# Optimization experiments

Measured on AMD Instinct MI355X. Metric: run time of the kernel, lower is better.

## Reference

```python
import jax, jax.numpy as jnp
import numpy as np

B, N, F_, CI, C, CO = 2, 1024, 2048, 3, 80, 128
NB = 15          # DirResNet blocks
Q = C // 4


def _graph_bn(x, g, b, eps=1e-5):
    # BatchNorm over channels with stats over (batch, nodes) -- training-mode batch stats
    mu = jnp.mean(x, axis=(0, 1), keepdims=True)
    var = jnp.var(x, axis=(0, 1), keepdims=True)
    return (x - mu) * jax.lax.rsqrt(var + eps) * g + b


def _graph_conv(L, x, W0, W1, bias):
    # GraphConv with k=1: linear on [x, L @ x]
    return x @ W0 + jnp.einsum('bnm,bmc->bnc', L, x) @ W1 + bias


def _forward(inputs, L, Di, DiA, mask,
             conv1_W0, conv1_W1, conv1_b,
             rn_bn0_g, rn_bn0_b, rn_fc0_W, rn_fc0_b,
             rn_bn1_g, rn_bn1_b, rn_fc1_W, rn_fc1_b,
             bn1_g, bn1_b, bn2_g, bn2_b, bn3_g, bn3_b,
             conv2_W0, conv2_W1, conv2_b):
    v = _graph_conv(L, inputs, conv1_W0, conv1_W1, conv1_b)      # [B,N,C]
    f = jnp.zeros((B, F_, C), v.dtype)
    z = jnp.zeros_like(v)
    carry = (f, f, v, z, z)  # [f, tmp_f, v, tmp_v, tmp_v]

    def block(carry, p):
        f, tmp_f, v, tv0, tv1 = carry
        g0, b0, W0, c0, g1, b1, W1, c1 = p
        # Dirac: vertices -> faces (quaternion reshape: [B,N,C] -> [B,4N,C/4])
        Dv = jnp.matmul(Di, v.reshape(B, 4 * N, Q)).reshape(B, F_, C)
        x = jnp.concatenate([f, Dv], axis=-1)                    # [B,F,2C]
        f_new = jax.nn.elu(_graph_bn(x, g0, b0) @ W0 + c0) + tmp_f
        # Adjoint Dirac: faces -> vertices
        Df = jnp.matmul(DiA, f_new.reshape(B, 4 * F_, Q)).reshape(B, N, C)
        y = jnp.concatenate([v, Df], axis=-1)                    # [B,N,2C]
        v_new = jax.nn.elu(_graph_bn(y, g1, b1) @ W1 + c1) + tv0
        return (f_new, f, v_new, v, tv0), None

    carry, _ = jax.lax.scan(
        block, carry,
        (rn_bn0_g, rn_bn0_b, rn_fc0_W, rn_fc0_b,
         rn_bn1_g, rn_bn1_b, rn_fc1_W, rn_fc1_b))
    _, _, v2, v1, v0 = carry
    v = jax.nn.elu(_graph_bn(v2, bn1_g, bn1_b)
                   + _graph_bn(v1, bn2_g, bn2_b)
                   + _graph_bn(v0, bn3_g, bn3_b))
    # Dropout2d: identity (eval mode / deterministic reference)
    v = _graph_conv(L, v, conv2_W0, conv2_W1, conv2_b)           # [B,N,CO]
    out = (v * mask).sum(axis=1) / mask.sum(axis=1)              # masked mean pool -> [B,CO]
    return out


def setup_inputs() -> dict:
    key = jax.random.key(0)
    ks = jax.random.split(key, 32)
    s = 0.05
    d = {
        'inputs': jax.random.normal(ks[0], (B, N, CI), jnp.float32),
        'L': jax.random.normal(ks[1], (B, N, N), jnp.float32) / np.float32(np.sqrt(N)),
        'Di': jax.random.normal(ks[2], (B, 4 * F_, 4 * N), jnp.float32) / np.float32(np.sqrt(4 * N)),
        'DiA': jax.random.normal(ks[3], (B, 4 * N, 4 * F_), jnp.float32) / np.float32(np.sqrt(4 * F_)),
        'mask': (jax.random.uniform(ks[4], (B, N, 1)) > 0.2).astype(jnp.float32),
        'conv1_W0': jax.random.normal(ks[5], (CI, C), jnp.float32) * s,
        'conv1_W1': jax.random.normal(ks[6], (CI, C), jnp.float32) * s,
        'conv1_b': jax.random.normal(ks[7], (C,), jnp.float32) * s,
        'rn_bn0_g': 1.0 + 0.1 * jax.random.normal(ks[8], (NB, 2 * C), jnp.float32),
        'rn_bn0_b': s * jax.random.normal(ks[9], (NB, 2 * C), jnp.float32),
        'rn_fc0_W': jax.random.normal(ks[10], (NB, 2 * C, C), jnp.float32) * s,
        'rn_fc0_b': jax.random.normal(ks[11], (NB, C), jnp.float32) * s,
        'rn_bn1_g': 1.0 + 0.1 * jax.random.normal(ks[12], (NB, 2 * C), jnp.float32),
        'rn_bn1_b': s * jax.random.normal(ks[13], (NB, 2 * C), jnp.float32),
        'rn_fc1_W': jax.random.normal(ks[14], (NB, 2 * C, C), jnp.float32) * s,
        'rn_fc1_b': jax.random.normal(ks[15], (NB, C), jnp.float32) * s,
        'bn1_g': 1.0 + 0.1 * jax.random.normal(ks[16], (C,), jnp.float32),
        'bn1_b': s * jax.random.normal(ks[17], (C,), jnp.float32),
        'bn2_g': 1.0 + 0.1 * jax.random.normal(ks[18], (C,), jnp.float32),
        'bn2_b': s * jax.random.normal(ks[19], (C,), jnp.float32),
        'bn3_g': 1.0 + 0.1 * jax.random.normal(ks[20], (C,), jnp.float32),
        'bn3_b': s * jax.random.normal(ks[21], (C,), jnp.float32),
        'conv2_W0': jax.random.normal(ks[22], (C, CO), jnp.float32) * s,
        'conv2_W1': jax.random.normal(ks[23], (C, CO), jnp.float32) * s,
        'conv2_b': jax.random.normal(ks[24], (CO,), jnp.float32) * s,
    }
    return d


def reference(inputs, L, Di, DiA, mask,
              conv1_W0, conv1_W1, conv1_b,
              rn_bn0_g, rn_bn0_b, rn_fc0_W, rn_fc0_b,
              rn_bn1_g, rn_bn1_b, rn_fc1_W, rn_fc1_b,
              bn1_g, bn1_b, bn2_g, bn2_b, bn3_g, bn3_b,
              conv2_W0, conv2_W1, conv2_b):
    return _forward(inputs, L, Di, DiA, mask,
                    conv1_W0, conv1_W1, conv1_b,
                    rn_bn0_g, rn_bn0_b, rn_fc0_W, rn_fc0_b,
                    rn_bn1_g, rn_bn1_b, rn_fc1_W, rn_fc1_b,
                    bn1_g, bn1_b, bn2_g, bn2_b, bn3_g, bn3_b,
                    conv2_W0, conv2_W1, conv2_b)
```

## Files before the change

kernel.cpp:

```cpp
#include <hip/hip_runtime.h>
#include <cstdint>

#define BB 2
#define NN 1024
#define FF 2048
#define CC 80
#define C2 160
#define NB_ 15
#define ROWS_X (BB*FF)
#define ROWS_Y (BB*NN)
#define WTP 168

typedef __attribute__((ext_vector_type(8))) _Float16 half8;
typedef __attribute__((ext_vector_type(4))) _Float16 half4;
typedef __attribute__((ext_vector_type(4))) float f32x4;

__device__ __forceinline__ void softbar() {
  __builtin_amdgcn_sched_barrier(0);
  asm volatile("s_waitcnt lgkmcnt(0)" ::: "memory");
  __builtin_amdgcn_s_barrier();
  __builtin_amdgcn_sched_barrier(0);
}

__global__ __launch_bounds__(256) void k_conv1(
    const float* __restrict__ inp, const float* __restrict__ L,
    const float* __restrict__ W0, const float* __restrict__ W1,
    const float* __restrict__ bias, float* __restrict__ v,
    float4* __restrict__ vstat)
{
  int bx = blockIdx.x;
  int b = bx >> 6, rb = bx & 63;
  int row0 = rb * 16;
  __shared__ float red[256][3];
  __shared__ float lx[16][3];
  __shared__ float st[16][2][CC];
  int t = threadIdx.x;
  int rloc = t >> 4, sl = t & 15;
  const float* Lrow = L + ((size_t)b*NN + row0 + rloc) * NN;
  const float* ipb  = inp + (size_t)b*NN*3;
  float a0=0.f,a1=0.f,a2=0.f;
  for (int m = sl; m < NN; m += 16) {
    float lv = Lrow[m];
    a0 = fmaf(lv, ipb[m*3+0], a0);
    a1 = fmaf(lv, ipb[m*3+1], a1);
    a2 = fmaf(lv, ipb[m*3+2], a2);
  }
  red[t][0]=a0; red[t][1]=a1; red[t][2]=a2;
  __syncthreads();
  if (t < 48) {
    int row = t/3, ci = t%3;
    float s=0.f;
    for (int s2=0; s2<16; ++s2) s += red[row*16+s2][ci];
    lx[row][ci]=s;
  }
  __syncthreads();
  for (int o = t; o < 16*CC; o += 256) {
    int row = o/CC, c = o%CC;
    const float* ir = inp + ((size_t)b*NN + row0 + row)*3;
    float val = bias[c];
    #pragma unroll
    for (int ci=0; ci<3; ++ci)
      val += ir[ci]*W0[ci*CC+c] + lx[row][ci]*W1[ci*CC+c];
    v[((size_t)b*NN + row0 + row)*CC + c] = val;
    st[row][0][c] = val;
    st[row][1][c] = val*val;
  }
  __syncthreads();
  if (t < 40) {
    float s0=0.f,q0=0.f,s1=0.f,q1=0.f;
    for (int row=0; row<16; ++row){
      s0+=st[row][0][2*t];   q0+=st[row][1][2*t];
      s1+=st[row][0][2*t+1]; q1+=st[row][1][2*t+1];
    }
    vstat[(size_t)bx*40 + t] = make_float4(s0,q0,s1,q1);
  }
}

__device__ __forceinline__ unsigned pkh(float a, float b){
  _Float16 ha = (_Float16)a, hb = (_Float16)b;
  unsigned short ua = __builtin_bit_cast(unsigned short, ha);
  unsigned short ub = __builtin_bit_cast(unsigned short, hb);
  return (unsigned)ua | ((unsigned)ub << 16);
}
__global__ __launch_bounds__(256) void k_cvt(
    const float* __restrict__ src, uint4* __restrict__ dst, size_t n8)
{
  size_t i = (size_t)blockIdx.x*256 + threadIdx.x;
  size_t stride = (size_t)gridDim.x*256;
  for (; i < n8; i += stride) {
    const float4* s = (const float4*)src + i*2;
    float4 f0 = s[0], f1 = s[1];
    uint4 o;
    o.x = pkh(f0.x,f0.y); o.y = pkh(f0.z,f0.w);
    o.z = pkh(f1.x,f1.y); o.w = pkh(f1.z,f1.w);
    dst[i] = o;
  }
}

__global__ __launch_bounds__(256) __attribute__((amdgpu_waves_per_eu(2,2)))
void k_dirac_mfma(
    const _Float16* __restrict__ A, const float* __restrict__ x,
    float* __restrict__ y, float4* __restrict__ stat, int M, int K)
{
  int b = blockIdx.y;
  A += (size_t)b*M*K; x += (size_t)b*(size_t)K*20; y += (size_t)b*(size_t)M*20;
  __shared__ _Float16 xT[2][2][32][264];
  __shared__ float cb_[2][8][64];
  __shared__ float stS[2][CC], stQ[2][CC];
  int t = threadIdx.x, lane = t & 63, w = t >> 6;
  int rw = w & 1, kh = w >> 1;
  int row0 = blockIdx.x*32 + rw*16;
  int cl = lane & 15, cg = lane >> 4;
  int KH = K >> 1;
  f32x4 acc0 = {0.f,0.f,0.f,0.f}, acc1 = {0.f,0.f,0.f,0.f};
  const float4* xv = (const float4*)x;
  int nchunk = KH >> 8;
  const _Float16* Abase = A + (size_t)(row0 + cl)*K + (size_t)kh*KH + cg*8;

  for (int i = t; i < 2*2*12*264; i += 256) {
    int bb = i / (2*12*264);
    int rem = i - bb*(2*12*264);
    int hh = rem / (12*264);
    int r2 = rem - hh*(12*264);
    xT[bb][hh][20 + r2/264][r2 % 264] = (_Float16)0.f;
  }
  {
    float4 s0[5], s1[5];
    #pragma unroll
    for (int i=0;i<5;++i){ s0[i]=xv[(size_t)t*5+i]; s1[i]=xv[((size_t)KH+t)*5+i]; }
    #pragma unroll
    for (int i=0;i<5;++i){
      xT[0][0][4*i+0][t]=(_Float16)s0[i].x; xT[0][0][4*i+1][t]=(_Float16)s0[i].y;
      xT[0][0][4*i+2][t]=(_Float16)s0[i].z; xT[0][0][4*i+3][t]=(_Float16)s0[i].w;
      xT[0][1][4*i+0][t]=(_Float16)s1[i].x; xT[0][1][4*i+1][t]=(_Float16)s1[i].y;
      xT[0][1][4*i+2][t]=(_Float16)s1[i].z; xT[0][1][4*i+3][t]=(_Float16)s1[i].w;
    }
  }
  half8 a_cur[8];
  #pragma unroll
  for (int ks=0;ks<8;++ks) a_cur[ks] = *(const half8*)(Abase + ks*32);
  __syncthreads();

  for (int c=0; c<nchunk; ++c) {
    int cur = c & 1;
    bool more = (c+1 < nchunk);
    float4 s0[5], s1[5];
    half8 a_nxt[8];
    if (more) {
      size_t k0 = (size_t)(c+1)*256 + t;
      #pragma unroll
      for (int i=0;i<5;++i){ s0[i]=xv[k0*5+i]; s1[i]=xv[(k0+KH)*5+i]; }
      const _Float16* An = Abase + (size_t)(c+1)*256;
      #pragma unroll
      for (int ks=0;ks<8;++ks) a_nxt[ks] = *(const half8*)(An + ks*32);
    }
    #pragma unroll
    for (int ks=0;ks<8;++ks) {
      half8 b0 = *(const half8*)(&xT[cur][kh][cl     ][ks*32 + cg*8]);
      half8 b1 = *(const half8*)(&xT[cur][kh][16 + cl][ks*32 + cg*8]);
      acc0 = __builtin_amdgcn_mfma_f32_16x16x32_f16(a_cur[ks], b0, acc0, 0,0,0);
      acc1 = __builtin_amdgcn_mfma_f32_16x16x32_f16(a_cur[ks], b1, acc1, 0,0,0);
    }
    if (more) {
      #pragma unroll
      for (int i=0;i<5;++i){
        xT[cur^1][0][4*i+0][t]=(_Float16)s0[i].x; xT[cur^1][0][4*i+1][t]=(_Float16)s0[i].y;
        xT[cur^1][0][4*i+2][t]=(_Float16)s0[i].z; xT[cur^1][0][4*i+3][t]=(_Float16)s0[i].w;
        xT[cur^1][1][4*i+0][t]=(_Float16)s1[i].x; xT[cur^1][1][4*i+1][t]=(_Float16)s1[i].y;
        xT[cur^1][1][4*i+2][t]=(_Float16)s1[i].z; xT[cur^1][1][4*i+3][t]=(_Float16)s1[i].w;
      }
      #pragma unroll
      for (int ks=0;ks<8;++ks) a_cur[ks] = a_nxt[ks];
    }
    softbar();
  }

  if (kh == 1) {
    #pragma unroll
    for (int j=0;j<4;++j){ cb_[rw][j][lane]=acc0[j]; cb_[rw][4+j][lane]=acc1[j]; }
  }
  __syncthreads();
  if (kh == 0) {
    #pragma unroll
    for (int j=0;j<4;++j){ acc0[j]+=cb_[rw][j][lane]; acc1[j]+=cb_[rw][4+j][lane]; }
    #pragma unroll
    for (int j=0;j<4;++j) {
      float v = acc0[j];
      y[(size_t)(row0 + 4*cg + j)*20 + cl] = v;
      float s = v, sq = v*v;
      s  += __shfl_xor(s,16);  s  += __shfl_xor(s,32);
      sq += __shfl_xor(sq,16); sq += __shfl_xor(sq,32);
      if (cg==0) { stS[rw][j*20+cl]=s; stQ[rw][j*20+cl]=sq; }
    }
    #pragma unroll
    for (int j=0;j<4;++j) {
      float v = acc1[j];
      if (cl < 4) y[(size_t)(row0 + 4*cg + j)*20 + 16 + cl] = v;
      float s = v, sq = v*v;
      s  += __shfl_xor(s,16);  s  += __shfl_xor(s,32);
      sq += __shfl_xor(sq,16); sq += __shfl_xor(sq,32);
      if (cg==0 && cl<4) { stS[rw][j*20+16+cl]=s; stQ[rw][j*20+16+cl]=sq; }
    }
  }
  __syncthreads();
  int slot = blockIdx.y*gridDim.x + blockIdx.x;
  if (t < 40) {
    float4 o;
    o.x = stS[0][2*t]  +stS[1][2*t];
    o.y = stQ[0][2*t]  +stQ[1][2*t];
    o.z = stS[0][2*t+1]+stS[1][2*t+1];
    o.w = stQ[0][2*t+1]+stQ[1][2*t+1];
    stat[(size_t)slot*40 + t] = o;
  }
}

__global__ __launch_bounds__(256) __attribute__((amdgpu_waves_per_eu(2,2)))
void k_dirac_f32(
    const float* __restrict__ A, const float* __restrict__ x,
    float* __restrict__ y, float4* __restrict__ stat, int M, int K)
{
  const int DR = 4;
  int b = blockIdx.y;
  A += (size_t)b*M*K; x += (size_t)b*(size_t)K*20; y += (size_t)b*(size_t)M*20;
  __shared__ float xs[2][20][256];
  __shared__ float stS[4][CC], stQ[4][CC];
  int t = threadIdx.x, lane = t & 63, w = t >> 6;
  int row0 = blockIdx.x*(4*DR) + w*DR;
  float acc[DR][20];
  #pragma unroll
  for (int r=0;r<DR;++r)
    #pragma unroll
    for (int q=0;q<20;++q) acc[r][q]=0.f;
  const float4* xv = (const float4*)x;
  int nchunk = K >> 8;
  const float* Abase = A + (size_t)row0*K + (lane<<2);
  {
    float4 s0[5];
    #pragma unroll
    for (int i=0;i<5;++i) s0[i] = xv[(size_t)t*5 + i];
    #pragma unroll
    for (int i=0;i<5;++i) {
      xs[0][4*i+0][t]=s0[i].x; xs[0][4*i+1][t]=s0[i].y;
      xs[0][4*i+2][t]=s0[i].z; xs[0][4*i+3][t]=s0[i].w;
    }
  }
  float4 a[DR];
  #pragma unroll
  for (int r=0;r<DR;++r) a[r] = *(const float4*)(Abase + (size_t)r*K);
  __syncthreads();
  for (int c=0; c<nchunk; ++c) {
    int cur = c & 1;
    bool more = (c+1 < nchunk);
    float4 st[5];
    if (more) {
      size_t kb = (size_t)(c+1)*256 + t;
      #pragma unroll
      for (int i=0;i<5;++i) st[i] = xv[kb*5 + i];
    }
    float4 af[DR];
    #pragma unroll
    for (int r=0;r<DR;++r) af[r] = a[r];
    if (more) {
      const float* An = Abase + (size_t)(c+1)*256;
      #pragma unroll
      for (int r=0;r<DR;++r) a[r] = *(const float4*)(An + (size_t)r*K);
    }
    #pragma unroll
    for (int q=0;q<20;++q) {
      float4 xq = *(const float4*)(&xs[cur][q][lane<<2]);
      #pragma unroll
      for (int r=0;r<DR;++r) {
        acc[r][q] = fmaf(af[r].x, xq.x, acc[r][q]);
        acc[r][q] = fmaf(af[r].y, xq.y, acc[r][q]);
        acc[r][q] = fmaf(af[r].z, xq.z, acc[r][q]);
        acc[r][q] = fmaf(af[r].w, xq.w, acc[r][q]);
      }
    }
    if (more) {
      #pragma unroll
      for (int i=0;i<5;++i) {
        xs[cur^1][4*i+0][t]=st[i].x; xs[cur^1][4*i+1][t]=st[i].y;
        xs[cur^1][4*i+2][t]=st[i].z; xs[cur^1][4*i+3][t]=st[i].w;
      }
    }
    __syncthreads();
  }
  #pragma unroll
  for (int r=0;r<DR;++r) {
    #pragma unroll
    for (int q=0;q<20;++q) {
      float s = acc[r][q];
      s += __shfl_xor(s, 1);  s += __shfl_xor(s, 2);
      s += __shfl_xor(s, 4);  s += __shfl_xor(s, 8);
      s += __shfl_xor(s, 16); s += __shfl_xor(s, 32);
      acc[r][q]=s;
    }
    if (lane==0) {
      float4* yp = (float4*)(y + (size_t)(row0+r)*20);
      yp[0] = make_float4(acc[r][0],acc[r][1],acc[r][2],acc[r][3]);
      yp[1] = make_float4(acc[r][4],acc[r][5],acc[r][6],acc[r][7]);
      yp[2] = make_float4(acc[r][8],acc[r][9],acc[r][10],acc[r][11]);
      yp[3] = make_float4(acc[r][12],acc[r][13],acc[r][14],acc[r][15]);
      yp[4] = make_float4(acc[r][16],acc[r][17],acc[r][18],acc[r][19]);
    }
  }
  if (lane == 0) {
    #pragma unroll
    for (int r=0;r<DR;++r)
      #pragma unroll
      for (int q=0;q<20;++q) {
        float v0 = acc[r][q];
        stS[w][r*20+q] = v0;
        stQ[w][r*20+q] = v0*v0;
      }
  }
  __syncthreads();
  int slot = blockIdx.y*gridDim.x + blockIdx.x;
  if (t < 40) {
    float4 o;
    o.x = stS[0][2*t]+stS[1][2*t]+stS[2][2*t]+stS[3][2*t];
    o.y = stQ[0][2*t]+stQ[1][2*t]+stQ[2][2*t]+stQ[3][2*t];
    o.z = stS[0][2*t+1]+stS[1][2*t+1]+stS[2][2*t+1]+stS[3][2*t+1];
    o.w = stQ[0][2*t+1]+stQ[1][2*t+1]+stQ[2][2*t+1]+stQ[3][2*t+1];
    stat[(size_t)slot*40 + t] = o;
  }
}

__global__ __launch_bounds__(320) void k_fc(
    const float* __restrict__ p1, const float* __restrict__ p2,
    const float4* __restrict__ sp1, int ns1,
    const float4* __restrict__ sp2, int ns2,
    const float* __restrict__ g, const float* __restrict__ bb,
    const float* __restrict__ W, const float* __restrict__ cb,
    const float* add, float* out,
    float4* __restrict__ statout, int rows, float invrows)
{
  __shared__ _Float16 Wt[80*WTP];
  __shared__ _Float16 xh[16*WTP];
  __shared__ float ad[2][C2];
  __shared__ float bpl[CC];
  __shared__ float4 pst[2][2][40];
  __shared__ float stS[CC], stQ[CC];
  int t = threadIdx.x;
  int lane = t & 63, wv = t >> 6;
  int cl = lane & 15, cg = lane >> 4;
  int r0 = blockIdx.x * 16;

  if (t < 160) {
    int p = t % 40, s = (t/40) & 1, h = t/80;
    const float4* sp = s ? sp2 : sp1;
    int ns = s ? ns2 : ns1;
    int half = ns >> 1;
    const float4* base = sp + (size_t)(h*half)*40 + p;
    float4 acc = {0.f,0.f,0.f,0.f};
    int i=0;
    for (; i+8<=half; i+=8) {
      float4 v[8];
      #pragma unroll
      for (int j=0;j<8;++j) v[j] = base[(size_t)(i+j)*40];
      #pragma unroll
      for (int j=0;j<8;++j){ acc.x+=v[j].x; acc.y+=v[j].y; acc.z+=v[j].z; acc.w+=v[j].w; }
    }
    for (; i<half; ++i){
      float4 v = base[(size_t)i*40];
      acc.x+=v.x; acc.y+=v.y; acc.z+=v.z; acc.w+=v.w;
    }
    pst[h][s][p] = acc;
  } else {
    int t2 = t - 160;
    #pragma unroll
    for (int i=0;i<20;++i) {
      int f4 = t2 + i*160;
      float4 w4 = ((const float4*)W)[f4];
      int c2 = f4/20, c = (f4%20)*4;
      Wt[(c+0)*WTP + c2] = (_Float16)w4.x;
      Wt[(c+1)*WTP + c2] = (_Float16)w4.y;
      Wt[(c+2)*WTP + c2] = (_Float16)w4.z;
      Wt[(c+3)*WTP + c2] = (_Float16)w4.w;
    }
  }
  __syncthreads();

  half8 bfr[5];
  #pragma unroll
  for (int ks=0;ks<5;++ks)
    bfr[ks] = *(const half8*)(&Wt[(wv*16+cl)*WTP + ks*32 + cg*8]);
  if (t < C2) {
    int s = (t < CC) ? 0 : 1;
    int chl = (t < CC) ? t : t - CC;
    int p = chl >> 1, e = chl & 1;
    float4 a0 = pst[0][s][p], a1 = pst[1][s][p];
    float S = e ? (a0.z + a1.z) : (a0.x + a1.x);
    float Q = e ? (a0.w + a1.w) : (a0.y + a1.y);
    float mean = S*invrows;
    float var  = fmaf(-mean, mean, Q*invrows);
    float aa   = g[t]*rsqrtf(var + 1e-5f);
    ad[0][t]=aa; ad[1][t]= bb[t] - mean*aa;
  }
  __syncthreads();

  #pragma unroll
  for (int i=0;i<2;++i) {
    int f4 = t + i*320;
    if (f4 < 640) {
      int row = f4/40, cq = (f4%40)*4;
      const float* src = (cq < 80) ? (p1 + (size_t)(r0+row)*CC + cq)
                                   : (p2 + (size_t)(r0+row)*CC + cq - 80);
      float4 x4 = *(const float4*)src;
      half4 h4;
      h4[0]=(_Float16)(x4.x*ad[0][cq+0]); h4[1]=(_Float16)(x4.y*ad[0][cq+1]);
      h4[2]=(_Float16)(x4.z*ad[0][cq+2]); h4[3]=(_Float16)(x4.w*ad[0][cq+3]);
      *(half4*)(&xh[row*WTP + cq]) = h4;
    }
  }
  if (t < CC) {
    float s = cb[t];
    #pragma unroll
    for (int ks=0;ks<20;++ks) {
      half8 w8 = *(const half8*)(&Wt[t*WTP + ks*8]);
      #pragma unroll
      for (int j=0;j<8;++j) s = fmaf(ad[1][ks*8+j], (float)w8[j], s);
    }
    bpl[t]=s;
  }
  __syncthreads();

  half8 afr[5];
  #pragma unroll
  for (int ks=0;ks<5;++ks)
    afr[ks] = *(const half8*)(&xh[cl*WTP + ks*32 + cg*8]);
  f32x4 acc = {0.f,0.f,0.f,0.f};
  #pragma unroll
  for (int ks=0;ks<5;++ks)
    acc = __builtin_amdgcn_mfma_f32_16x16x32_f16(afr[ks], bfr[ks], acc, 0,0,0);
  float ss=0.f, sq=0.f;
  int col = wv*16 + cl;
  #pragma unroll
  for (int j=0;j<4;++j) {
    int row = r0 + 4*cg + j;
    float val = acc[j] + bpl[col];
    val = val>0.f ? val : expm1f(val);
    val += add[(size_t)row*CC + col];
    out[(size_t)row*CC + col] = val;
    ss += val; sq = fmaf(val,val,sq);
  }
  ss += __shfl_xor(ss,16); ss += __shfl_xor(ss,32);
  sq += __shfl_xor(sq,16); sq += __shfl_xor(sq,32);
  if (cg==0) { stS[col]=ss; stQ[col]=sq; }
  __syncthreads();
  if (t < 40)
    statout[(size_t)blockIdx.x*40 + t] = make_float4(stS[2*t], stQ[2*t], stS[2*t+1], stQ[2*t+1]);
}

__global__ __launch_bounds__(256) void k_final(
    const float* __restrict__ v2, const float* __restrict__ v1, const float* __restrict__ v0,
    const float4* __restrict__ s2, const float4* __restrict__ s1, const float4* __restrict__ s0,
    const float* __restrict__ g1, const float* __restrict__ b1,
    const float* __restrict__ g2, const float* __restrict__ b2,
    const float* __restrict__ g3, const float* __restrict__ b3,
    float* __restrict__ vf, int ns)
{
  __shared__ float A[3][CC], D[3][CC];
  __shared__ float4 pf[2][3][40];
  int t = threadIdx.x;
  if (t < 240) {
    int p = t % 40, s = (t/40) % 3, h = t/120;
    const float4* sp = s==0 ? s2 : (s==1 ? s1 : s0);
    int half = ns >> 1;
    const float4* base = sp + (size_t)(h*half)*40 + p;
    float4 acc = {0.f,0.f,0.f,0.f};
    int i=0;
    for (; i+8<=half; i+=8) {
      float4 v[8];
      #pragma unroll
      for (int j=0;j<8;++j) v[j] = base[(size_t)(i+j)*40];
      #pragma unroll
      for (int j=0;j<8;++j){ acc.x+=v[j].x; acc.y+=v[j].y; acc.z+=v[j].z; acc.w+=v[j].w; }
    }
    for (; i<half; ++i){
      float4 v = base[(size_t)i*40];
      acc.x+=v.x; acc.y+=v.y; acc.z+=v.z; acc.w+=v.w;
    }
    pf[h][s][p] = acc;
  }
  __syncthreads();
  if (t < 240) {
    int set = t/80, chl = t%80, p = chl>>1, e = chl&1;
    const float* gg  = set==0? g1 : (set==1? g2 : g3);
    const float* bbp = set==0? b1 : (set==1? b2 : b3);
    float4 a0 = pf[0][set][p], a1 = pf[1][set][p];
    float S = e ? (a0.z + a1.z) : (a0.x + a1.x);
    float Q = e ? (a0.w + a1.w) : (a0.y + a1.y);
    float mean = S*(1.f/ROWS_Y);
    float var  = fmaf(-mean,mean,Q*(1.f/ROWS_Y));
    float aa   = gg[chl]*rsqrtf(var+1e-5f);
    A[set][chl]=aa; D[set][chl]=bbp[chl]-mean*aa;
  }
  __syncthreads();
  for (size_t idx = (size_t)blockIdx.x*256 + t; idx < (size_t)ROWS_Y*CC; idx += (size_t)gridDim.x*256) {
    int c = (int)(idx % CC);
    float val = fmaf(v2[idx],A[0][c],D[0][c]) + fmaf(v1[idx],A[1][c],D[1][c]) + fmaf(v0[idx],A[2][c],D[2][c]);
    vf[idx] = val>0.f? val : expm1f(val);
  }
}

__global__ __launch_bounds__(256) void k_w(
    const float* __restrict__ mask, const float* __restrict__ L, float* __restrict__ w)
{
  int bx = blockIdx.x;
  int b = bx >> 4, n0 = (bx & 15) * 64;
  int t = threadIdx.x;
  int ks = t >> 6;
  __shared__ float red[4][64];
  float acc=0.f;
  const float* Lb = L + (size_t)b*NN*NN;
  const float* mb = mask + b*NN;
  int n = n0 + (t & 63);
  for (int k = ks*256; k < ks*256+256; k+=8) {
    float mv[8], lv[8];
    #pragma unroll
    for (int j=0;j<8;++j){ mv[j]=mb[k+j]; lv[j]=Lb[(size_t)(k+j)*NN + n]; }
    #pragma unroll
    for (int j=0;j<8;++j) acc = fmaf(mv[j], lv[j], acc);
  }
  red[ks][t&63]=acc;
  __syncthreads();
  if (t < 64) w[b*NN + n0 + t] = red[0][t]+red[1][t]+red[2][t]+red[3][t];
}

__global__ __launch_bounds__(256) void k_pool(
    const float* __restrict__ vf, const float* __restrict__ mask,
    const float* __restrict__ w, float* __restrict__ part)
{
  int bx = blockIdx.x;
  int b = bx >> 3, slab = bx & 7;
  int t = threadIdx.x, c = t%CC, rs = t/CC;
  __shared__ float st[3][2][CC];
  if (t<240) {
    float a1=0.f,a2=0.f;
    for (int r = rs; r < 128; r += 3) {
      int row = slab*128 + r;
      float val = vf[((size_t)b*NN + row)*CC + c];
      a1 = fmaf(mask[b*NN+row], val, a1);
      a2 = fmaf(w[b*NN+row],    val, a2);
    }
    st[rs][0][c]=a1; st[rs][1][c]=a2;
  }
  __syncthreads();
  if (t<CC) {
    part[((b*8+slab)*2+0)*CC+t] = st[0][0][t]+st[1][0][t]+st[2][0][t];
    part[((b*8+slab)*2+1)*CC+t] = st[0][1][t]+st[1][1][t]+st[2][1][t];
  }
}

__global__ __launch_bounds__(256) void k_out(
    const float* __restrict__ part, const float* __restrict__ mask,
    const float* __restrict__ W0, const float* __restrict__ W1,
    const float* __restrict__ b2, float* __restrict__ outp)
{
  __shared__ float pl[2][2][CC];
  __shared__ float msred[2][128];
  __shared__ float ms[2];
  int t = threadIdx.x;
  {
    int b = t >> 7, k0 = t & 127;
    float m[8];
    #pragma unroll
    for (int j=0;j<8;++j) m[j] = mask[b*NN + k0 + j*128];
    msred[b][k0] = ((m[0]+m[1])+(m[2]+m[3]))+((m[4]+m[5])+(m[6]+m[7]));
  }
  if (t < 160) {
    int b = t/CC, c = t%CC;
    float v1[8], v2[8];
    #pragma unroll
    for (int slab=0; slab<8; ++slab){
      v1[slab] = part[((b*8+slab)*2+0)*CC+c];
      v2[slab] = part[((b*8+slab)*2+1)*CC+c];
    }
    float s1=0.f,s2=0.f;
    #pragma unroll
    for (int slab=0;slab<8;++slab){ s1+=v1[slab]; s2+=v2[slab]; }
    pl[b][0][c]=s1; pl[b][1][c]=s2;
  }
  __syncthreads();
  if (t < 2) {
    float s=0.f;
    for (int k=0;k<128;++k) s += msred[t][k];
    ms[t]=s;
  }
  __syncthreads();
  int b = t >> 7, co = t & 127;
  float acc = 0.f;
  for (int c=0;c<CC;c+=8) {
    float w0[8], w1[8];
    #pragma unroll
    for (int j=0;j<8;++j){ w0[j]=W0[(c+j)*128+co]; w1[j]=W1[(c+j)*128+co]; }
    #pragma unroll
    for (int j=0;j<8;++j) acc += pl[b][0][c+j]*w0[j] + pl[b][1][c+j]*w1[j];
  }
  outp[t] = acc/ms[b] + b2[co];
}

extern "C" void kernel_launch(void* const* d_in, const int* in_sizes, int n_in,
                              void* d_out, int out_size, void* d_ws, size_t ws_size,
                              hipStream_t stream)
{
  const float* inp  = (const float*)d_in[0];
  const float* L    = (const float*)d_in[1];
  const float* Di   = (const float*)d_in[2];
  const float* DiA  = (const float*)d_in[3];
  const float* mask = (const float*)d_in[4];
  const float* c1W0 = (const float*)d_in[5];
  const float* c1W1 = (const float*)d_in[6];
  const float* c1b  = (const float*)d_in[7];
  const float* bn0g = (const float*)d_in[8];
  const float* bn0b = (const float*)d_in[9];
  const float* fc0W = (const float*)d_in[10];
  const float* fc0b = (const float*)d_in[11];
  const float* bn1g = (const float*)d_in[12];
  const float* bn1b = (const float*)d_in[13];
  const float* fc1W = (const float*)d_in[14];
  const float* fc1b = (const float*)d_in[15];
  const float* fbn1g= (const float*)d_in[16];
  const float* fbn1b= (const float*)d_in[17];
  const float* fbn2g= (const float*)d_in[18];
  const float* fbn2b= (const float*)d_in[19];
  const float* fbn3g= (const float*)d_in[20];
  const float* fbn3b= (const float*)d_in[21];
  const float* c2W0 = (const float*)d_in[22];
  const float* c2W1 = (const float*)d_in[23];
  const float* c2b  = (const float*)d_in[24];

  float* ws = (float*)d_ws;
  size_t off = 0;
  auto alloc = [&](size_t n)->float* { float* p = ws + off; off += (n + 63) & ~(size_t)63; return p; };
  const size_t STFL = (size_t)1024*40*4;
  float* vb[3];   for (int i=0;i<3;++i) vb[i]   = alloc((size_t)BB*NN*CC);
  float* fb[2];   for (int i=0;i<2;++i) fb[i]   = alloc((size_t)BB*FF*CC);
  float* Dv       = alloc((size_t)BB*FF*CC);
  float* Df       = alloc((size_t)BB*NN*CC);
  float4* vstat[3];for (int i=0;i<3;++i) vstat[i]= (float4*)alloc(STFL);
  float4* fstat[2];for (int i=0;i<2;++i) fstat[i]= (float4*)alloc(STFL);
  float4* dvstat  = (float4*)alloc(STFL);
  float4* dfstat  = (float4*)alloc(STFL);
  float* vf       = alloc((size_t)BB*NN*CC);
  float* wv       = alloc((size_t)BB*NN);
  float* part     = alloc((size_t)16*2*CC);
  const size_t nDi = (size_t)BB*(4*FF)*(4*NN);
  _Float16* Dih  = (_Float16*)alloc(nDi/2);
  _Float16* DiAh = (_Float16*)alloc(nDi/2);
  bool usebf = (off*sizeof(float) <= ws_size);

  hipMemsetAsync(fb[0],    0, (size_t)BB*FF*CC*4, stream);
  hipMemsetAsync(fb[1],    0, (size_t)BB*FF*CC*4, stream);
  hipMemsetAsync(vb[1],    0, (size_t)BB*NN*CC*4, stream);
  hipMemsetAsync(fstat[0], 0, (size_t)256*40*16, stream);

  if (usebf) {
    k_cvt<<<4096,256,0,stream>>>(Di,  (uint4*)Dih,  nDi/8);
    k_cvt<<<4096,256,0,stream>>>(DiA, (uint4*)DiAh, nDi/8);
  }

  k_conv1<<<128,256,0,stream>>>(inp, L, c1W0, c1W1, c1b, vb[0], vstat[0]);

  int nsDv = usebf ? 512 : 1024;
  int nsDf = usebf ? 256 : 512;
  int cur=0, p1=1, p2=2, fcur=0, fs=0;
  for (int it=0; it<NB_; ++it) {
    if (usebf) k_dirac_mfma<<<dim3(256,2),256,0,stream>>>(Dih, vb[cur], Dv, dvstat, 4*FF, 4*NN);
    else       k_dirac_f32 <<<dim3(512,2),256,0,stream>>>(Di,  vb[cur], Dv, dvstat, 4*FF, 4*NN);
    k_fc<<<ROWS_X/16,320,0,stream>>>(fb[fcur], Dv, fstat[fs],256, dvstat,nsDv,
        bn0g+(size_t)it*C2, bn0b+(size_t)it*C2, fc0W+(size_t)it*C2*CC, fc0b+(size_t)it*CC,
        fb[1-fcur], fb[1-fcur], fstat[1-fs], ROWS_X, 1.f/ROWS_X);
    fcur = 1-fcur; fs = 1-fs;
    if (usebf) k_dirac_mfma<<<dim3(128,2),256,0,stream>>>(DiAh, fb[fcur], Df, dfstat, 4*NN, 4*FF);
    else       k_dirac_f32 <<<dim3(256,2),256,0,stream>>>(DiA,  fb[fcur], Df, dfstat, 4*NN, 4*FF);
    k_fc<<<ROWS_Y/16,320,0,stream>>>(vb[cur], Df, vstat[cur],128, dfstat,nsDf,
        bn1g+(size_t)it*C2, bn1b+(size_t)it*C2, fc1W+(size_t)it*C2*CC, fc1b+(size_t)it*CC,
        vb[p1], vb[p2], vstat[p2], ROWS_Y, 1.f/ROWS_Y);
    int tmp=p2; p2=p1; p1=cur; cur=tmp;
  }

  k_final<<<128,256,0,stream>>>(vb[cur],vb[p1],vb[p2], vstat[cur],vstat[p1],vstat[p2],
      fbn1g,fbn1b,fbn2g,fbn2b,fbn3g,fbn3b, vf, 128);
  k_w<<<32,256,0,stream>>>(mask, L, wv);
  k_pool<<<16,256,0,stream>>>(vf, mask, wv, part);
  k_out<<<1,256,0,stream>>>(part, mask, c2W0, c2W1, c2b, (float*)d_out);
}
```

Before: 1.966 ms.

## Fuse fp32-to-fp16 Dirac conversion into first MFMA pass and widen adjoint grid

Drops the two standalone conversion kernels. On the first block iteration the Dirac MFMA kernel reads the fp32 operator directly, converts it to fp16 in registers, uses it, and writes the fp16 copy back for later iterations. The adjoint Dirac kernel is templated to use 128-thread blocks holding a single 16-row tile, which doubles its grid so more CUs are busy, and the stats slot count is updated to match. In exchange the first iteration loses the register prefetch of A (loads are synchronous) and has to read fp32 and write fp16 in-line.

```diff
diff --git a/kernel.cpp b/kernel.cpp
--- a/kernel.cpp
+++ b/kernel.cpp
@@ -76,48 +76,35 @@
   }
 }
 
-__device__ __forceinline__ unsigned pkh(float a, float b){
-  _Float16 ha = (_Float16)a, hb = (_Float16)b;
-  unsigned short ua = __builtin_bit_cast(unsigned short, ha);
-  unsigned short ub = __builtin_bit_cast(unsigned short, hb);
-  return (unsigned)ua | ((unsigned)ub << 16);
-}
-__global__ __launch_bounds__(256) void k_cvt(
-    const float* __restrict__ src, uint4* __restrict__ dst, size_t n8)
-{
-  size_t i = (size_t)blockIdx.x*256 + threadIdx.x;
-  size_t stride = (size_t)gridDim.x*256;
-  for (; i < n8; i += stride) {
-    const float4* s = (const float4*)src + i*2;
-    float4 f0 = s[0], f1 = s[1];
-    uint4 o;
-    o.x = pkh(f0.x,f0.y); o.y = pkh(f0.z,f0.w);
-    o.z = pkh(f1.x,f1.y); o.w = pkh(f1.z,f1.w);
-    dst[i] = o;
-  }
-}
-
-__global__ __launch_bounds__(256) __attribute__((amdgpu_waves_per_eu(2,2)))
+template<int WR, bool CVT>
+__global__ __launch_bounds__(WR*128) __attribute__((amdgpu_waves_per_eu(2,2)))
 void k_dirac_mfma(
-    const _Float16* __restrict__ A, const float* __restrict__ x,
+    const void* __restrict__ Ain, _Float16* __restrict__ Aout,
+    const float* __restrict__ x,
     float* __restrict__ y, float4* __restrict__ stat, int M, int K)
 {
+  constexpr int NT  = WR*128;
+  constexpr int RPT = 256/NT;
   int b = blockIdx.y;
-  A += (size_t)b*M*K; x += (size_t)b*(size_t)K*20; y += (size_t)b*(size_t)M*20;
+  x += (size_t)b*(size_t)K*20; y += (size_t)b*(size_t)M*20;
+  const _Float16* Ah = (const _Float16*)Ain + (size_t)b*M*K;
+  const float*    Af = (const float*)Ain    + (size_t)b*M*K;
+  _Float16* Ao = CVT ? (Aout + (size_t)b*M*K) : nullptr;
   __shared__ _Float16 xT[2][2][32][264];
-  __shared__ float cb_[2][8][64];
-  __shared__ float stS[2][CC], stQ[2][CC];
+  __shared__ float cb_[WR][8][64];
+  __shared__ float stS[WR][CC], stQ[WR][CC];
   int t = threadIdx.x, lane = t & 63, w = t >> 6;
-  int rw = w & 1, kh = w >> 1;
-  int row0 = blockIdx.x*32 + rw*16;
+  int rw = (WR==2) ? (w & 1) : 0;
+  int kh = (WR==2) ? (w >> 1) : w;
+  int row0 = blockIdx.x*(16*WR) + rw*16;
   int cl = lane & 15, cg = lane >> 4;
   int KH = K >> 1;
   f32x4 acc0 = {0.f,0.f,0.f,0.f}, acc1 = {0.f,0.f,0.f,0.f};
   const float4* xv = (const float4*)x;
   int nchunk = KH >> 8;
-  const _Float16* Abase = A + (size_t)(row0 + cl)*K + (size_t)kh*KH + cg*8;
-
-  for (int i = t; i < 2*2*12*264; i += 256) {
+  size_t aoff = (size_t)(row0 + cl)*K + (size_t)kh*KH + cg*8;
+
+  for (int i = t; i < 2*2*12*264; i += NT) {
     int bb = i / (2*12*264);
     int rem = i - bb*(2*12*264);
     int hh = rem / (12*264);
@@ -125,34 +112,68 @@
     xT[bb][hh][20 + r2/264][r2 % 264] = (_Float16)0.f;
   }
   {
-    float4 s0[5], s1[5];
-    #pragma unroll
-    for (int i=0;i<5;++i){ s0[i]=xv[(size_t)t*5+i]; s1[i]=xv[((size_t)KH+t)*5+i]; }
-    #pragma unroll
-    for (int i=0;i<5;++i){
-      xT[0][0][4*i+0][t]=(_Float16)s0[i].x; xT[0][0][4*i+1][t]=(_Float16)s0[i].y;
-      xT[0][0][4*i+2][t]=(_Float16)s0[i].z; xT[0][0][4*i+3][t]=(_Float16)s0[i].w;
-      xT[0][1][4*i+0][t]=(_Float16)s1[i].x; xT[0][1][4*i+1][t]=(_Float16)s1[i].y;
-      xT[0][1][4*i+2][t]=(_Float16)s1[i].z; xT[0][1][4*i+3][t]=(_Float16)s1[i].w;
-    }
+    float4 s[2][RPT][5];
+    #pragma unroll
+    for (int h=0;h<2;++h)
+      #pragma unroll
+      for (int r=0;r<RPT;++r) {
+        size_t kr = (size_t)(h?KH:0) + t + r*NT;
+        #pragma unroll
+        for (int i=0;i<5;++i) s[h][r][i] = xv[kr*5+i];
+      }
+    #pragma unroll
+    for (int h=0;h<2;++h)
+      #pragma unroll
+      for (int r=0;r<RPT;++r) {
+        int kr = t + r*NT;
+        #pragma unroll
+        for (int i=0;i<5;++i){
+          xT[0][h][4*i+0][kr]=(_Float16)s[h][r][i].x;
+          xT[0][h][4*i+1][kr]=(_Float16)s[h][r][i].y;
+          xT[0][h][4*i+2][kr]=(_Float16)s[h][r][i].z;
+          xT[0][h][4*i+3][kr]=(_Float16)s[h][r][i].w;
+        }
+      }
   }
   half8 a_cur[8];
-  #pragma unroll
-  for (int ks=0;ks<8;++ks) a_cur[ks] = *(const half8*)(Abase + ks*32);
+  if constexpr (!CVT) {
+    #pragma unroll
+    for (int ks=0;ks<8;++ks) a_cur[ks] = *(const half8*)(Ah + aoff + ks*32);
+  }
   __syncthreads();
 
   for (int c=0; c<nchunk; ++c) {
     int cur = c & 1;
     bool more = (c+1 < nchunk);
-    float4 s0[5], s1[5];
+    float4 s[2][RPT][5];
     half8 a_nxt[8];
     if (more) {
-      size_t k0 = (size_t)(c+1)*256 + t;
-      #pragma unroll
-      for (int i=0;i<5;++i){ s0[i]=xv[k0*5+i]; s1[i]=xv[(k0+KH)*5+i]; }
-      const _Float16* An = Abase + (size_t)(c+1)*256;
-      #pragma unroll
-      for (int ks=0;ks<8;++ks) a_nxt[ks] = *(const half8*)(An + ks*32);
+      #pragma unroll
+      for (int h=0;h<2;++h)
+        #pragma unroll
+        for (int r=0;r<RPT;++r) {
+          size_t kr = (size_t)(h?KH:0) + (size_t)(c+1)*256 + t + r*NT;
+          #pragma unroll
+          for (int i=0;i<5;++i) s[h][r][i] = xv[kr*5+i];
+        }
+      if constexpr (!CVT) {
+        const _Float16* An = Ah + aoff + (size_t)(c+1)*256;
+        #pragma unroll
+        for (int ks=0;ks<8;++ks) a_nxt[ks] = *(const half8*)(An + ks*32);
+      }
+    }
+    if constexpr (CVT) {
+      size_t ao = aoff + (size_t)c*256;
+      #pragma unroll
+      for (int ks=0;ks<8;++ks) {
+        float4 f0 = *(const float4*)(Af + ao + ks*32);
+        float4 f1 = *(const float4*)(Af + ao + ks*32 + 4);
+        half8 a;
+        a[0]=(_Float16)f0.x; a[1]=(_Float16)f0.y; a[2]=(_Float16)f0.z; a[3]=(_Float16)f0.w;
+        a[4]=(_Float16)f1.x; a[5]=(_Float16)f1.y; a[6]=(_Float16)f1.z; a[7]=(_Float16)f1.w;
+        a_cur[ks] = a;
+        *(half8*)(Ao + ao + ks*32) = a;
+      }
     }
     #pragma unroll
     for (int ks=0;ks<8;++ks) {
@@ -163,14 +184,22 @@
     }
     if (more) {
       #pragma unroll
-      for (int i=0;i<5;++i){
-        xT[cur^1][0][4*i+0][t]=(_Float16)s0[i].x; xT[cur^1][0][4*i+1][t]=(_Float16)s0[i].y;
-        xT[cur^1][0][4*i+2][t]=(_Float16)s0[i].z; xT[cur^1][0][4*i+3][t]=(_Float16)s0[i].w;
-        xT[cur^1][1][4*i+0][t]=(_Float16)s1[i].x; xT[cur^1][1][4*i+1][t]=(_Float16)s1[i].y;
-        xT[cur^1][1][4*i+2][t]=(_Float16)s1[i].z; xT[cur^1][1][4*i+3][t]=(_Float16)s1[i].w;
+      for (int h=0;h<2;++h)
+        #pragma unroll
+        for (int r=0;r<RPT;++r) {
+          int kr = t + r*NT;
+          #pragma unroll
+          for (int i=0;i<5;++i){
+            xT[cur^1][h][4*i+0][kr]=(_Float16)s[h][r][i].x;
+            xT[cur^1][h][4*i+1][kr]=(_Float16)s[h][r][i].y;
+            xT[cur^1][h][4*i+2][kr]=(_Float16)s[h][r][i].z;
+            xT[cur^1][h][4*i+3][kr]=(_Float16)s[h][r][i].w;
+          }
+        }
+      if constexpr (!CVT) {
+        #pragma unroll
+        for (int ks=0;ks<8;++ks) a_cur[ks] = a_nxt[ks];
       }
-      #pragma unroll
-      for (int ks=0;ks<8;++ks) a_cur[ks] = a_nxt[ks];
     }
     softbar();
   }
@@ -205,11 +234,12 @@
   __syncthreads();
   int slot = blockIdx.y*gridDim.x + blockIdx.x;
   if (t < 40) {
-    float4 o;
-    o.x = stS[0][2*t]  +stS[1][2*t];
-    o.y = stQ[0][2*t]  +stQ[1][2*t];
-    o.z = stS[0][2*t+1]+stS[1][2*t+1];
-    o.w = stQ[0][2*t+1]+stQ[1][2*t+1];
+    float4 o = {0.f,0.f,0.f,0.f};
+    #pragma unroll
+    for (int r=0;r<WR;++r){
+      o.x += stS[r][2*t];   o.y += stQ[r][2*t];
+      o.z += stS[r][2*t+1]; o.w += stQ[r][2*t+1];
+    }
     stat[(size_t)slot*40 + t] = o;
   }
 }
@@ -656,26 +686,29 @@
   hipMemsetAsync(vb[1],    0, (size_t)BB*NN*CC*4, stream);
   hipMemsetAsync(fstat[0], 0, (size_t)256*40*16, stream);
 
-  if (usebf) {
-    k_cvt<<<4096,256,0,stream>>>(Di,  (uint4*)Dih,  nDi/8);
-    k_cvt<<<4096,256,0,stream>>>(DiA, (uint4*)DiAh, nDi/8);
-  }
-
   k_conv1<<<128,256,0,stream>>>(inp, L, c1W0, c1W1, c1b, vb[0], vstat[0]);
 
   int nsDv = usebf ? 512 : 1024;
-  int nsDf = usebf ? 256 : 512;
+  int nsDf = usebf ? 512 : 512;
   int cur=0, p1=1, p2=2, fcur=0, fs=0;
   for (int it=0; it<NB_; ++it) {
-    if (usebf) k_dirac_mfma<<<dim3(256,2),256,0,stream>>>(Dih, vb[cur], Dv, dvstat, 4*FF, 4*NN);
-    else       k_dirac_f32 <<<dim3(512,2),256,0,stream>>>(Di,  vb[cur], Dv, dvstat, 4*FF, 4*NN);
+    if (usebf) {
+      if (it==0) k_dirac_mfma<2,true ><<<dim3(256,2),256,0,stream>>>(Di,  Dih, vb[cur], Dv, dvstat, 4*FF, 4*NN);
+      else       k_dirac_mfma<2,false><<<dim3(256,2),256,0,stream>>>(Dih, Dih, vb[cur], Dv, dvstat, 4*FF, 4*NN);
+    } else {
+      k_dirac_f32<<<dim3(512,2),256,0,stream>>>(Di, vb[cur], Dv, dvstat, 4*FF, 4*NN);
+    }
     k_fc<<<ROWS_X/16,320,0,stream>>>(fb[fcur], Dv, fstat[fs],256, dvstat,nsDv,
         bn0g+(size_t)it*C2, bn0b+(size_t)it*C2, fc0W+(size_t)it*C2*CC, fc0b+(size_t)it*CC,
         fb[1-fcur], fb[1-fcur], fstat[1-fs], ROWS_X, 1.f/ROWS_X);
     fcur = 1-fcur; fs = 1-fs;
-    if (usebf) k_dirac_mfma<<<dim3(128,2),256,0,stream>>>(DiAh, fb[fcur], Df, dfstat, 4*NN, 4*FF);
-    else       k_dirac_f32 <<<dim3(256,2),256,0,stream>>>(DiA,  fb[fcur], Df, dfstat, 4*NN, 4*FF);
-    k_fc<<<ROWS_Y/16,320,0,stream>>>(vb[cur], Df, vstat[cur],128, dfstat,nsDf,
+    if (usebf) {
+      if (it==0) k_dirac_mfma<1,true ><<<dim3(256,2),128,0,stream>>>(DiA,  DiAh, fb[fcur], Df, dfstat, 4*NN, 4*FF);
+      else       k_dirac_mfma<1,false><<<dim3(256,2),128,0,stream>>>(DiAh, DiAh, fb[fcur], Df, dfstat, 4*NN, 4*FF);
+    } else {
+      k_dirac_f32<<<dim3(256,2),256,0,stream>>>(DiA, fb[fcur], Df, dfstat, 4*NN, 4*FF);
+    }
+    k_fc<<<ROWS_Y/16,320,0,stream>>>(vb[cur], Df, vstat[cur],(it==0?128:128), dfstat,nsDf,
         bn1g+(size_t)it*C2, bn1b+(size_t)it*C2, fc1W+(size_t)it*C2*CC, fc1b+(size_t)it*CC,
         vb[p1], vb[p2], vstat[p2], ROWS_Y, 1.f/ROWS_Y);
     int tmp=p2; p2=p1; p1=cur; cur=tmp;
```

After: 2.074 ms. 5.5% more time.
